# Kernel tuning notes

Measured on AMD Instinct MI355X. Metric: run time of the kernel, lower is better.

Reference implementation:

```python
import jax, jax.numpy as jnp
import numpy as np

N = 16384          # number of vectors to quantize (flattened leading dims)
K = 2 ** 14        # codebook_size = 2**bits_per_codeword
D = 64             # vector_dim


def setup_inputs() -> dict:
    key = jax.random.key(0)
    k1, k2, k3, k4 = jax.random.split(key, 4)
    x_re = jax.random.normal(k1, (N, D), dtype=jnp.float32)
    x_im = jax.random.normal(k2, (N, D), dtype=jnp.float32)
    # random complex codebook, normalized so each row has unit complex L2 norm
    cb_re = jax.random.normal(k3, (K, D), dtype=jnp.float32)
    cb_im = jax.random.normal(k4, (K, D), dtype=jnp.float32)
    norm = jnp.sqrt(jnp.sum(cb_re * cb_re + cb_im * cb_im, axis=1, keepdims=True))
    cb_re = cb_re / norm
    cb_im = cb_im / norm
    return {"x_re": x_re, "x_im": x_im, "cb_re": cb_re, "cb_im": cb_im}


def reference(x_re, x_im, cb_re, cb_im):
    # complex inner product conj(x) . c, expanded in real arithmetic:
    #   Re = x_re.c_re + x_im.c_im ;  Im = x_re.c_im - x_im.c_re
    dot_re = jnp.einsum('nd,kd->nk', x_re, cb_re) + jnp.einsum('nd,kd->nk', x_im, cb_im)
    dot_im = jnp.einsum('nd,kd->nk', x_re, cb_im) - jnp.einsum('nd,kd->nk', x_im, cb_re)
    mag = jnp.sqrt(dot_re * dot_re + dot_im * dot_im)  # [N, K] abs of complex dot
    indices = jnp.argmax(mag, axis=-1)                 # [N] int
    # reconstruction: gather codebook rows (call() with int input)
    recon = jnp.stack([cb_re[indices], cb_im[indices]], axis=-1)  # [N, D, 2] (re, im)
    return indices, recon
```

## Files before the change

### kernel.cpp

```cpp
#include <hip/hip_runtime.h>

#define NROWS 16384
#define KCB   16384
#define DD    64
#define BM    256
#define CSPLIT 16
#define COLS_PER_BLOCK 1024
#define TILE_COLS 128
#define NTILES (COLS_PER_BLOCK / TILE_COLS)
#define NCHUNK (TILE_COLS / 16)
#define CAP 2048
#define DELTA 0.45f
#define TILE_BYTES 32768

typedef __attribute__((ext_vector_type(8))) short bf16x8;
typedef __attribute__((ext_vector_type(4))) float f32x4;
typedef __attribute__((ext_vector_type(2))) float f32x2;

__device__ __forceinline__ unsigned pk_bf16(float lo, float hi) {
    unsigned a = __float_as_uint(lo);
    unsigned b = __float_as_uint(hi);
    a += 0x7FFFu + ((a >> 16) & 1u);
    b += 0x7FFFu + ((b >> 16) & 1u);
    return (a >> 16) | (b & 0xFFFF0000u);
}

__device__ __forceinline__ bf16x8 mk8(unsigned a, unsigned b, unsigned c, unsigned d) {
    union { uint4 u; bf16x8 v; } x;
    x.u = make_uint4(a, b, c, d);
    return x.v;
}

__device__ __forceinline__ f32x2 lo2(f32x4 v) { return __builtin_shufflevector(v, v, 0, 1); }
__device__ __forceinline__ f32x2 hi2(f32x4 v) { return __builtin_shufflevector(v, v, 2, 3); }

__device__ __forceinline__ unsigned swz(unsigned row, unsigned byte_in_row) {
    return row * 128u + (byte_in_row ^ ((row & 7u) << 4));
}

__device__ __forceinline__ void gload_lds16(const void* g, void* l) {
    __builtin_amdgcn_global_load_lds(
        (__attribute__((address_space(1))) void*)(g),
        (__attribute__((address_space(3))) void*)(l), 16, 0, 0);
}

__device__ __forceinline__ void rescore_fast(
    int n, int k,
    const float* __restrict__ x_re, const float* __restrict__ x_im,
    const float* __restrict__ cb_re, const float* __restrict__ cb_im,
    unsigned long long* __restrict__ best_packed)
{
    const float4* xr = (const float4*)(x_re + (size_t)n * DD);
    const float4* xi = (const float4*)(x_im + (size_t)n * DD);
    const float4* cr = (const float4*)(cb_re + (size_t)k * DD);
    const float4* ci = (const float4*)(cb_im + (size_t)k * DD);
    float accr = 0.0f, acci = 0.0f;
#pragma unroll 4
    for (int d4 = 0; d4 < 16; ++d4) {
        float4 a = xr[d4], b = xi[d4], c = cr[d4], e = ci[d4];
        accr = fmaf(a.x, c.x, accr); accr = fmaf(b.x, e.x, accr);
        acci = fmaf(a.x, e.x, acci); acci = fmaf(-b.x, c.x, acci);
        accr = fmaf(a.y, c.y, accr); accr = fmaf(b.y, e.y, accr);
        acci = fmaf(a.y, e.y, acci); acci = fmaf(-b.y, c.y, acci);
        accr = fmaf(a.z, c.z, accr); accr = fmaf(b.z, e.z, accr);
        acci = fmaf(a.z, e.z, acci); acci = fmaf(-b.z, c.z, acci);
        accr = fmaf(a.w, c.w, accr); accr = fmaf(b.w, e.w, accr);
        acci = fmaf(a.w, e.w, acci); acci = fmaf(-b.w, c.w, acci);
    }
    float m2 = accr * accr + acci * acci;
    unsigned long long key =
        ((unsigned long long)__float_as_uint(m2) << 32) | (unsigned)(~(unsigned)k);
    atomicMax(best_packed + n, key);
}

__global__ __launch_bounds__(256) void prep(
    const float* __restrict__ cb_re, const float* __restrict__ cb_im,
    uint4* __restrict__ cb_sw,
    unsigned* __restrict__ row_max_bits,
    unsigned long long* __restrict__ best_packed, int* __restrict__ flags)
{
    int id = blockIdx.x * 256 + threadIdx.x;
    if (id < NROWS) { row_max_bits[id] = 0u; best_packed[id] = 0ull; }
    if (id < 1024) flags[id] = 0;
    int u   = id & 1023;
    int arr = (id >> 10) & 1;
    int gt  = id >> 11;
    int c   = u >> 3;
    int b   = ((u & 7) * 16) ^ ((c & 7) << 4);
    int col = gt * TILE_COLS + c;
    int d0  = b >> 1;
    const float* src = arr ? cb_im : cb_re;
    const float4* p = (const float4*)(src + (size_t)col * DD + d0);
    float4 f0 = p[0], f1 = p[1];
    cb_sw[id] = make_uint4(pk_bf16(f0.x, f0.y), pk_bf16(f0.z, f0.w),
                           pk_bf16(f1.x, f1.y), pk_bf16(f1.z, f1.w));
}

template<int PASS>
__global__ __launch_bounds__(512, 2) void score_kernel(
    const float* __restrict__ x_re, const float* __restrict__ x_im,
    const float* __restrict__ cb_re, const float* __restrict__ cb_im,
    const char* __restrict__ cb_sw,
    unsigned* __restrict__ row_max_bits,
    unsigned long long* __restrict__ best_packed, int* __restrict__ flags)
{
    __shared__ char Bls[2][2][TILE_COLS * 128];
    __shared__ unsigned cand[CAP];
    __shared__ int cand_cnt;

    const int tid  = threadIdx.x;
    const int lane = tid & 63;
    const int wid  = tid >> 6;
    const int row0 = blockIdx.x * BM;
    const int col0 = blockIdx.y * COLS_PER_BLOCK;
    const int bid  = blockIdx.y * gridDim.x + blockIdx.x;
    const int l15  = lane & 15;
    const int lhi  = lane >> 4;

    if (tid == 0) cand_cnt = 0;

    bf16x8 Ar[2][2], Ai[2][2], Ain[2][2];
#pragma unroll
    for (int a = 0; a < 2; ++a) {
        const int row = row0 + wid * 32 + a * 16 + l15;
#pragma unroll
        for (int ks = 0; ks < 2; ++ks) {
            const float4* pr = (const float4*)(x_re + (size_t)row * DD + ks * 32 + lhi * 8);
            const float4* pi = (const float4*)(x_im + (size_t)row * DD + ks * 32 + lhi * 8);
            float4 r0 = pr[0], r1 = pr[1];
            float4 i0 = pi[0], i1 = pi[1];
            Ar[a][ks] = mk8(pk_bf16(r0.x, r0.y), pk_bf16(r0.z, r0.w),
                            pk_bf16(r1.x, r1.y), pk_bf16(r1.z, r1.w));
            Ai[a][ks] = mk8(pk_bf16(i0.x, i0.y), pk_bf16(i0.z, i0.w),
                            pk_bf16(i1.x, i1.y), pk_bf16(i1.z, i1.w));
            Ain[a][ks] = Ai[a][ks] ^ (short)0x8000;
        }
    }

    const f32x4 FZERO = (f32x4){0.f, 0.f, 0.f, 0.f};

    f32x2 rm2[2][2];
    f32x2 thr2[2][2];
#pragma unroll
    for (int a = 0; a < 2; ++a)
#pragma unroll
        for (int j = 0; j < 2; ++j) rm2[a][j] = (f32x2){0.f, 0.f};
    if (PASS == 2) {
#pragma unroll
        for (int a = 0; a < 2; ++a)
#pragma unroll
            for (int j = 0; j < 2; ++j) {
#pragma unroll
                for (int h = 0; h < 2; ++h) {
                    int n = row0 + wid * 32 + a * 16 + lhi * 4 + j * 2 + h;
                    float mx = __uint_as_float(row_max_bits[n]);
                    float tm = sqrtf(mx) - DELTA;
                    thr2[a][j][h] = (tm > 0.0f) ? tm * tm : -1.0f;
                }
            }
    }

    bool ovf = false;

    const char* tile_base = cb_sw + (size_t)blockIdx.y * NTILES * TILE_BYTES;
    auto stage = [&](int buf, int t) {
        const char* src = tile_base + (size_t)t * TILE_BYTES;
        char* dst = &Bls[buf][0][0];
#pragma unroll
        for (int j = 0; j < 4; ++j)
            gload_lds16(src + j * 8192 + tid * 16, dst + j * 8192 + tid * 16);
    };

    stage(0, 0);
    __syncthreads();

    for (int t = 0; t < NTILES; ++t) {
        const int cur = t & 1;
        if (t + 1 < NTILES) {
            stage(cur ^ 1, t + 1);
            asm volatile("s_waitcnt vmcnt(4)" ::: "memory");
        } else {
            asm volatile("s_waitcnt vmcnt(0)" ::: "memory");
        }
        __builtin_amdgcn_sched_barrier(0);
        __builtin_amdgcn_s_barrier();
        __builtin_amdgcn_sched_barrier(0);

        for (int ch = 0; ch < NCHUNK; ++ch) {
            const char* B0 = &Bls[cur][0][0];
            const char* B1 = &Bls[cur][1][0];
            const int colLocal = ch * 16 + l15;
            unsigned off0 = swz(colLocal, lhi * 16);
            unsigned off1 = swz(colLocal, 64 + lhi * 16);
            bf16x8 br0 = *(const bf16x8*)(B0 + off0);
            bf16x8 bi0 = *(const bf16x8*)(B1 + off0);
            bf16x8 br1 = *(const bf16x8*)(B0 + off1);
            bf16x8 bi1 = *(const bf16x8*)(B1 + off1);

            f32x4 accre[2], accim[2];
#pragma unroll
            for (int a = 0; a < 2; ++a) {
                accre[a] = __builtin_amdgcn_mfma_f32_16x16x32_bf16(Ar[a][0], br0, FZERO, 0, 0, 0);
                accre[a] = __builtin_amdgcn_mfma_f32_16x16x32_bf16(Ai[a][0], bi0, accre[a], 0, 0, 0);
                accre[a] = __builtin_amdgcn_mfma_f32_16x16x32_bf16(Ar[a][1], br1, accre[a], 0, 0, 0);
                accre[a] = __builtin_amdgcn_mfma_f32_16x16x32_bf16(Ai[a][1], bi1, accre[a], 0, 0, 0);
                accim[a] = __builtin_amdgcn_mfma_f32_16x16x32_bf16(Ar[a][0], bi0, FZERO, 0, 0, 0);
                accim[a] = __builtin_amdgcn_mfma_f32_16x16x32_bf16(Ain[a][0], br0, accim[a], 0, 0, 0);
                accim[a] = __builtin_amdgcn_mfma_f32_16x16x32_bf16(Ar[a][1], bi1, accim[a], 0, 0, 0);
                accim[a] = __builtin_amdgcn_mfma_f32_16x16x32_bf16(Ain[a][1], br1, accim[a], 0, 0, 0);
            }

#pragma unroll
            for (int a = 0; a < 2; ++a) {
                f32x2 m2p[2];
                {
                    f32x2 rl = lo2(accre[a]), il = lo2(accim[a]);
                    f32x2 rh = hi2(accre[a]), ih = hi2(accim[a]);
                    m2p[0] = rl * rl + il * il;
                    m2p[1] = rh * rh + ih * ih;
                }
                if (PASS == 1) {
#pragma unroll
                    for (int j = 0; j < 2; ++j)
                        rm2[a][j] = __builtin_elementwise_max(rm2[a][j], m2p[j]);
                } else {
#pragma unroll
                    for (int j = 0; j < 2; ++j)
#pragma unroll
                        for (int h = 0; h < 2; ++h) {
                            if (m2p[j][h] >= thr2[a][j][h]) {
                                int nl = wid * 32 + a * 16 + lhi * 4 + j * 2 + h;
                                int k  = col0 + t * TILE_COLS + ch * 16 + l15;
                                int idx = atomicAdd(&cand_cnt, 1);
                                if (idx < CAP) cand[idx] = ((unsigned)nl << 14) | (unsigned)k;
                                else ovf = true;
                            }
                        }
                }
            }
        }

        __builtin_amdgcn_sched_barrier(0);
        __builtin_amdgcn_s_barrier();
    }
    __syncthreads();

    if (PASS == 1) {
#pragma unroll
        for (int a = 0; a < 2; ++a)
#pragma unroll
            for (int j = 0; j < 2; ++j)
#pragma unroll
                for (int h = 0; h < 2; ++h) {
                    float v = rm2[a][j][h];
#pragma unroll
                    for (int m = 1; m < 16; m <<= 1)
                        v = fmaxf(v, __shfl_xor(v, m, 64));
                    if (l15 == 0) {
                        int n = row0 + wid * 32 + a * 16 + lhi * 4 + j * 2 + h;
                        atomicMax(&row_max_bits[n], __float_as_uint(v));
                    }
                }
    } else {
        if (ovf) flags[bid] = 1;
        int cnt = cand_cnt < CAP ? cand_cnt : CAP;
        for (int i = tid; i < cnt; i += 512) {
            unsigned e = cand[i];
            rescore_fast(row0 + (int)(e >> 14), (int)(e & 16383u),
                         x_re, x_im, cb_re, cb_im, best_packed);
        }
    }
}

__global__ __launch_bounds__(512) void rescue(
    const float* __restrict__ x_re, const float* __restrict__ x_im,
    const float* __restrict__ cb_re, const float* __restrict__ cb_im,
    const int* __restrict__ flags,
    unsigned long long* __restrict__ best_packed)
{
    const int bid = blockIdx.x;
    if (flags[bid] == 0) return;
    const int row0 = (bid & 63) * BM;
    const int col0 = (bid >> 6) * COLS_PER_BLOCK;
    for (int i = threadIdx.x; i < BM * COLS_PER_BLOCK; i += 512)
        rescore_fast(row0 + (i >> 10), col0 + (i & 1023),
                     x_re, x_im, cb_re, cb_im, best_packed);
}

__global__ __launch_bounds__(256) void finalize(
    const unsigned long long* __restrict__ best_packed,
    const float* __restrict__ cb_re, const float* __restrict__ cb_im,
    float* __restrict__ out)
{
    const int wave = threadIdx.x >> 6;
    const int lane = threadIdx.x & 63;
    const int n = blockIdx.x * 4 + wave;
    if (n >= NROWS) return;

    unsigned long long p = best_packed[n];
    unsigned k = ~(unsigned)(p & 0xFFFFFFFFull);

    if (lane == 0) out[n] = (float)k;

    float re = cb_re[(size_t)k * DD + lane];
    float im = cb_im[(size_t)k * DD + lane];
    float2* ro = reinterpret_cast<float2*>(out + NROWS);
    ro[(size_t)n * DD + lane] = make_float2(re, im);
}

extern "C" void kernel_launch(void* const* d_in, const int* in_sizes, int n_in,
                              void* d_out, int out_size, void* d_ws, size_t ws_size,
                              hipStream_t stream)
{
    const float* x_re  = (const float*)d_in[0];
    const float* x_im  = (const float*)d_in[1];
    const float* cb_re = (const float*)d_in[2];
    const float* cb_im = (const float*)d_in[3];
    float* out = (float*)d_out;

    const size_t CB_SW_BYTES = (size_t)(KCB / TILE_COLS) * TILE_BYTES;
    char* p = (char*)d_ws;
    const char* cb_sw = p;                                        p += CB_SW_BYTES;
    unsigned long long* best_packed = (unsigned long long*)p;     p += (size_t)NROWS * 8;
    unsigned* row_max_bits = (unsigned*)p;                        p += (size_t)NROWS * 4;
    int* flags = (int*)p;

    prep<<<1024, 256, 0, stream>>>(cb_re, cb_im, (uint4*)d_ws,
                                   row_max_bits, best_packed, flags);

    dim3 grid(NROWS / BM, CSPLIT);
    score_kernel<1><<<grid, 512, 0, stream>>>(x_re, x_im, cb_re, cb_im, cb_sw,
                                              row_max_bits, best_packed, flags);
    score_kernel<2><<<grid, 512, 0, stream>>>(x_re, x_im, cb_re, cb_im, cb_sw,
                                              row_max_bits, best_packed, flags);

    rescue<<<1024, 512, 0, stream>>>(x_re, x_im, cb_re, cb_im, flags, best_packed);

    finalize<<<NROWS / 4, 256, 0, stream>>>(best_packed, cb_re, cb_im, out);
}
```

Baseline: 295.8 us.

## Replace full max pass with sampled estimate kernel over a subset of codebook tiles

Drops the first full scoring pass, which computed each row's exact max magnitude over the whole codebook. A small est_kernel now computes a lower-bound estimate of that max from 8 codebook tiles. The single scoring pass then filters candidates against a threshold derived from this estimate. This roughly halves the MFMA work, but the looser threshold lets many more candidates through to the fp32 rescoring. It also raises the risk of overflowing the candidate buffer, which triggers the expensive rescue path.

```diff
diff --git a/kernel.cpp b/kernel.cpp
--- a/kernel.cpp
+++ b/kernel.cpp
@@ -9,13 +9,13 @@
 #define TILE_COLS 128
 #define NTILES (COLS_PER_BLOCK / TILE_COLS)
 #define NCHUNK (TILE_COLS / 16)
+#define EST_TILES 8
 #define CAP 2048
 #define DELTA 0.45f
 #define TILE_BYTES 32768
 
 typedef __attribute__((ext_vector_type(8))) short bf16x8;
 typedef __attribute__((ext_vector_type(4))) float f32x4;
-typedef __attribute__((ext_vector_type(2))) float f32x2;
 
 __device__ __forceinline__ unsigned pk_bf16(float lo, float hi) {
     unsigned a = __float_as_uint(lo);
@@ -30,9 +30,6 @@
     x.u = make_uint4(a, b, c, d);
     return x.v;
 }
-
-__device__ __forceinline__ f32x2 lo2(f32x4 v) { return __builtin_shufflevector(v, v, 0, 1); }
-__device__ __forceinline__ f32x2 hi2(f32x4 v) { return __builtin_shufflevector(v, v, 2, 3); }
 
 __device__ __forceinline__ unsigned swz(unsigned row, unsigned byte_in_row) {
     return row * 128u + (byte_in_row ^ ((row & 7u) << 4));
@@ -76,11 +73,11 @@
 __global__ __launch_bounds__(256) void prep(
     const float* __restrict__ cb_re, const float* __restrict__ cb_im,
     uint4* __restrict__ cb_sw,
-    unsigned* __restrict__ row_max_bits,
+    unsigned* __restrict__ row_est,
     unsigned long long* __restrict__ best_packed, int* __restrict__ flags)
 {
     int id = blockIdx.x * 256 + threadIdx.x;
-    if (id < NROWS) { row_max_bits[id] = 0u; best_packed[id] = 0ull; }
+    if (id < NROWS) { row_est[id] = 0u; best_packed[id] = 0ull; }
     if (id < 1024) flags[id] = 0;
     int u   = id & 1023;
     int arr = (id >> 10) & 1;
@@ -96,30 +93,21 @@
                            pk_bf16(f1.x, f1.y), pk_bf16(f1.z, f1.w));
 }
 
-template<int PASS>
-__global__ __launch_bounds__(512, 2) void score_kernel(
+__global__ __launch_bounds__(512, 2) void est_kernel(
     const float* __restrict__ x_re, const float* __restrict__ x_im,
-    const float* __restrict__ cb_re, const float* __restrict__ cb_im,
     const char* __restrict__ cb_sw,
-    unsigned* __restrict__ row_max_bits,
-    unsigned long long* __restrict__ best_packed, int* __restrict__ flags)
-{
-    __shared__ char Bls[2][2][TILE_COLS * 128];
-    __shared__ unsigned cand[CAP];
-    __shared__ int cand_cnt;
+    unsigned* __restrict__ row_est)
+{
+    __shared__ char Bls[2][TILE_COLS * 128];
 
     const int tid  = threadIdx.x;
     const int lane = tid & 63;
     const int wid  = tid >> 6;
     const int row0 = blockIdx.x * BM;
-    const int col0 = blockIdx.y * COLS_PER_BLOCK;
-    const int bid  = blockIdx.y * gridDim.x + blockIdx.x;
     const int l15  = lane & 15;
     const int lhi  = lane >> 4;
 
-    if (tid == 0) cand_cnt = 0;
-
-    bf16x8 Ar[2][2], Ai[2][2], Ain[2][2];
+    bf16x8 Ar[2][2], Ai[2][2];
 #pragma unroll
     for (int a = 0; a < 2; ++a) {
         const int row = row0 + wid * 32 + a * 16 + l15;
@@ -133,32 +121,142 @@
                             pk_bf16(r1.x, r1.y), pk_bf16(r1.z, r1.w));
             Ai[a][ks] = mk8(pk_bf16(i0.x, i0.y), pk_bf16(i0.z, i0.w),
                             pk_bf16(i1.x, i1.y), pk_bf16(i1.z, i1.w));
-            Ain[a][ks] = Ai[a][ks] ^ (short)0x8000;
-        }
-    }
-
-    const f32x4 FZERO = (f32x4){0.f, 0.f, 0.f, 0.f};
-
-    f32x2 rm2[2][2];
-    f32x2 thr2[2][2];
+        }
+    }
+
+    {
+        const char* src = cb_sw + (size_t)blockIdx.y * TILE_BYTES;
+        char* dst = &Bls[0][0];
+#pragma unroll
+        for (int j = 0; j < 4; ++j)
+            gload_lds16(src + j * 8192 + tid * 16, dst + j * 8192 + tid * 16);
+    }
+    __syncthreads();
+
+    float rm[2][4];
 #pragma unroll
     for (int a = 0; a < 2; ++a)
 #pragma unroll
-        for (int j = 0; j < 2; ++j) rm2[a][j] = (f32x2){0.f, 0.f};
-    if (PASS == 2) {
+        for (int r = 0; r < 4; ++r) rm[a][r] = 0.0f;
+
+    for (int ch = 0; ch < NCHUNK; ++ch) {
+        const char* B0 = &Bls[0][0];
+        const char* B1 = &Bls[1][0];
+        const int colLocal = ch * 16 + l15;
+        unsigned off0 = swz(colLocal, lhi * 16);
+        unsigned off1 = swz(colLocal, 64 + lhi * 16);
+        bf16x8 br0 = *(const bf16x8*)(B0 + off0);
+        bf16x8 bi0 = *(const bf16x8*)(B1 + off0);
+        bf16x8 br1 = *(const bf16x8*)(B0 + off1);
+        bf16x8 bi1 = *(const bf16x8*)(B1 + off1);
+
+        f32x4 accre[2], accim[2];
+#pragma unroll
+        for (int a = 0; a < 2; ++a) {
+            accre[a] = (f32x4){0.f, 0.f, 0.f, 0.f};
+            accim[a] = (f32x4){0.f, 0.f, 0.f, 0.f};
+        }
+#pragma unroll
+        for (int a = 0; a < 2; ++a) {
+            accre[a] = __builtin_amdgcn_mfma_f32_16x16x32_bf16(Ar[a][0], br0, accre[a], 0, 0, 0);
+            accre[a] = __builtin_amdgcn_mfma_f32_16x16x32_bf16(Ai[a][0], bi0, accre[a], 0, 0, 0);
+            accre[a] = __builtin_amdgcn_mfma_f32_16x16x32_bf16(Ar[a][1], br1, accre[a], 0, 0, 0);
+            accre[a] = __builtin_amdgcn_mfma_f32_16x16x32_bf16(Ai[a][1], bi1, accre[a], 0, 0, 0);
+            accim[a] = __builtin_amdgcn_mfma_f32_16x16x32_bf16(Ar[a][0], bi0, accim[a], 0, 0, 0);
+            accim[a] = __builtin_amdgcn_mfma_f32_16x16x32_bf16(Ar[a][1], bi1, accim[a], 0, 0, 0);
+        }
+        br0 = br0 ^ (short)0x8000;
+        br1 = br1 ^ (short)0x8000;
+#pragma unroll
+        for (int a = 0; a < 2; ++a) {
+            accim[a] = __builtin_amdgcn_mfma_f32_16x16x32_bf16(Ai[a][0], br0, accim[a], 0, 0, 0);
+            accim[a] = __builtin_amdgcn_mfma_f32_16x16x32_bf16(Ai[a][1], br1, accim[a], 0, 0, 0);
+        }
 #pragma unroll
         for (int a = 0; a < 2; ++a)
 #pragma unroll
-            for (int j = 0; j < 2; ++j) {
-#pragma unroll
-                for (int h = 0; h < 2; ++h) {
-                    int n = row0 + wid * 32 + a * 16 + lhi * 4 + j * 2 + h;
-                    float mx = __uint_as_float(row_max_bits[n]);
-                    float tm = sqrtf(mx) - DELTA;
-                    thr2[a][j][h] = (tm > 0.0f) ? tm * tm : -1.0f;
-                }
+            for (int r = 0; r < 4; ++r) {
+                float re = accre[a][r], im = accim[a][r];
+                rm[a][r] = fmaxf(rm[a][r], fmaf(re, re, im * im));
             }
     }
+
+#pragma unroll
+    for (int m = 1; m < 16; m <<= 1)
+#pragma unroll
+        for (int a = 0; a < 2; ++a)
+#pragma unroll
+            for (int r = 0; r < 4; ++r)
+                rm[a][r] = fmaxf(rm[a][r], __shfl_xor(rm[a][r], m, 64));
+    if (l15 == 0) {
+#pragma unroll
+        for (int a = 0; a < 2; ++a)
+#pragma unroll
+            for (int r = 0; r < 4; ++r) {
+                int n = row0 + wid * 32 + a * 16 + lhi * 4 + r;
+                atomicMax(&row_est[n], __float_as_uint(rm[a][r]));
+            }
+    }
+}
+
+__global__ __launch_bounds__(512, 2) void score_kernel(
+    const float* __restrict__ x_re, const float* __restrict__ x_im,
+    const float* __restrict__ cb_re, const float* __restrict__ cb_im,
+    const char* __restrict__ cb_sw,
+    const unsigned* __restrict__ row_est,
+    unsigned long long* __restrict__ best_packed, int* __restrict__ flags)
+{
+    __shared__ char Bls[2][2][TILE_COLS * 128];
+    __shared__ unsigned cand[CAP];
+    __shared__ int cand_cnt;
+
+    const int tid  = threadIdx.x;
+    const int lane = tid & 63;
+    const int wid  = tid >> 6;
+    const int row0 = blockIdx.x * BM;
+    const int col0 = blockIdx.y * COLS_PER_BLOCK;
+    const int bid  = blockIdx.y * gridDim.x + blockIdx.x;
+    const int l15  = lane & 15;
+    const int lhi  = lane >> 4;
+
+    if (tid == 0) cand_cnt = 0;
+
+    bf16x8 Ar[2][2], Ai[2][2];
+#pragma unroll
+    for (int a = 0; a < 2; ++a) {
+        const int row = row0 + wid * 32 + a * 16 + l15;
+        {
+            const float4* pr = (const float4*)(x_re + (size_t)row * DD + lhi * 8);
+            const float4* pi = (const float4*)(x_im + (size_t)row * DD + lhi * 8);
+            float4 r0 = pr[0], r1 = pr[1];
+            float4 i0 = pi[0], i1 = pi[1];
+            Ar[a][0] = mk8(pk_bf16(r0.x, r0.y), pk_bf16(r0.z, r0.w),
+                           pk_bf16(r1.x, r1.y), pk_bf16(r1.z, r1.w));
+            Ai[a][0] = mk8(pk_bf16(i0.x, i0.y), pk_bf16(i0.z, i0.w),
+                           pk_bf16(i1.x, i1.y), pk_bf16(i1.z, i1.w));
+        }
+        {
+            const float4* pr = (const float4*)(x_re + (size_t)row * DD + 32 + lhi * 8);
+            const float4* pi = (const float4*)(x_im + (size_t)row * DD + 32 + lhi * 8);
+            float4 r0 = pr[0], r1 = pr[1];
+            float4 i0 = pi[0], i1 = pi[1];
+            Ar[a][1] = mk8(pk_bf16(r0.x, r0.y), pk_bf16(r0.z, r0.w),
+                           pk_bf16(r1.x, r1.y), pk_bf16(r1.z, r1.w));
+            Ai[a][1] = mk8(pk_bf16(i0.x, i0.y), pk_bf16(i0.z, i0.w),
+                           pk_bf16(i1.x, i1.y), pk_bf16(i1.z, i1.w));
+        }
+    }
+
+    float thr[2][4];
+#pragma unroll
+    for (int a = 0; a < 2; ++a)
+#pragma unroll
+        for (int r = 0; r < 4; ++r) {
+            int n = row0 + wid * 32 + a * 16 + lhi * 4 + r;
+            float mx = __uint_as_float(row_est[n]);
+            float tm = sqrtf(mx) - DELTA;
+            thr[a][r] = (tm > 0.0f) ? tm * tm : -1.0f;
+        }
 
     bool ovf = false;
 
@@ -200,44 +298,40 @@
             f32x4 accre[2], accim[2];
 #pragma unroll
             for (int a = 0; a < 2; ++a) {
-                accre[a] = __builtin_amdgcn_mfma_f32_16x16x32_bf16(Ar[a][0], br0, FZERO, 0, 0, 0);
+                accre[a] = (f32x4){0.f, 0.f, 0.f, 0.f};
+                accim[a] = (f32x4){0.f, 0.f, 0.f, 0.f};
+            }
+#pragma unroll
+            for (int a = 0; a < 2; ++a) {
+                accre[a] = __builtin_amdgcn_mfma_f32_16x16x32_bf16(Ar[a][0], br0, accre[a], 0, 0, 0);
                 accre[a] = __builtin_amdgcn_mfma_f32_16x16x32_bf16(Ai[a][0], bi0, accre[a], 0, 0, 0);
                 accre[a] = __builtin_amdgcn_mfma_f32_16x16x32_bf16(Ar[a][1], br1, accre[a], 0, 0, 0);
                 accre[a] = __builtin_amdgcn_mfma_f32_16x16x32_bf16(Ai[a][1], bi1, accre[a], 0, 0, 0);
-                accim[a] = __builtin_amdgcn_mfma_f32_16x16x32_bf16(Ar[a][0], bi0, FZERO, 0, 0, 0);
-                accim[a] = __builtin_amdgcn_mfma_f32_16x16x32_bf16(Ain[a][0], br0, accim[a], 0, 0, 0);
+                accim[a] = __builtin_amdgcn_mfma_f32_16x16x32_bf16(Ar[a][0], bi0, accim[a], 0, 0, 0);
                 accim[a] = __builtin_amdgcn_mfma_f32_16x16x32_bf16(Ar[a][1], bi1, accim[a], 0, 0, 0);
-                accim[a] = __builtin_amdgcn_mfma_f32_16x16x32_bf16(Ain[a][1], br1, accim[a], 0, 0, 0);
             }
-
+            br0 = br0 ^ (short)0x8000;
+            br1 = br1 ^ (short)0x8000;
 #pragma unroll
             for (int a = 0; a < 2; ++a) {
-                f32x2 m2p[2];
-                {
-                    f32x2 rl = lo2(accre[a]), il = lo2(accim[a]);
-                    f32x2 rh = hi2(accre[a]), ih = hi2(accim[a]);
-                    m2p[0] = rl * rl + il * il;
-                    m2p[1] = rh * rh + ih * ih;
+                accim[a] = __builtin_amdgcn_mfma_f32_16x16x32_bf16(Ai[a][0], br0, accim[a], 0, 0, 0);
+                accim[a] = __builtin_amdgcn_mfma_f32_16x16x32_bf16(Ai[a][1], br1, accim[a], 0, 0, 0);
+            }
+
+#pragma unroll
+            for (int a = 0; a < 2; ++a)
+#pragma unroll
+                for (int r = 0; r < 4; ++r) {
+                    float re = accre[a][r], im = accim[a][r];
+                    float m2 = fmaf(re, re, im * im);
+                    if (m2 >= thr[a][r]) {
+                        int nl = wid * 32 + a * 16 + lhi * 4 + r;
+                        int k  = col0 + t * TILE_COLS + ch * 16 + l15;
+                        int idx = atomicAdd(&cand_cnt, 1);
+                        if (idx < CAP) cand[idx] = ((unsigned)nl << 14) | (unsigned)k;
+                        else ovf = true;
+                    }
                 }
-                if (PASS == 1) {
-#pragma unroll
-                    for (int j = 0; j < 2; ++j)
-                        rm2[a][j] = __builtin_elementwise_max(rm2[a][j], m2p[j]);
-                } else {
-#pragma unroll
-                    for (int j = 0; j < 2; ++j)
-#pragma unroll
-                        for (int h = 0; h < 2; ++h) {
-                            if (m2p[j][h] >= thr2[a][j][h]) {
-                                int nl = wid * 32 + a * 16 + lhi * 4 + j * 2 + h;
-                                int k  = col0 + t * TILE_COLS + ch * 16 + l15;
-                                int idx = atomicAdd(&cand_cnt, 1);
-                                if (idx < CAP) cand[idx] = ((unsigned)nl << 14) | (unsigned)k;
-                                else ovf = true;
-                            }
-                        }
-                }
-            }
         }
 
         __builtin_amdgcn_sched_barrier(0);
@@ -245,30 +339,12 @@
     }
     __syncthreads();
 
-    if (PASS == 1) {
-#pragma unroll
-        for (int a = 0; a < 2; ++a)
-#pragma unroll
-            for (int j = 0; j < 2; ++j)
-#pragma unroll
-                for (int h = 0; h < 2; ++h) {
-                    float v = rm2[a][j][h];
-#pragma unroll
-                    for (int m = 1; m < 16; m <<= 1)
-                        v = fmaxf(v, __shfl_xor(v, m, 64));
-                    if (l15 == 0) {
-                        int n = row0 + wid * 32 + a * 16 + lhi * 4 + j * 2 + h;
-                        atomicMax(&row_max_bits[n], __float_as_uint(v));
-                    }
-                }
-    } else {
-        if (ovf) flags[bid] = 1;
-        int cnt = cand_cnt < CAP ? cand_cnt : CAP;
-        for (int i = tid; i < cnt; i += 512) {
-            unsigned e = cand[i];
-            rescore_fast(row0 + (int)(e >> 14), (int)(e & 16383u),
-                         x_re, x_im, cb_re, cb_im, best_packed);
-        }
+    if (ovf) flags[bid] = 1;
+    int cnt = cand_cnt < CAP ? cand_cnt : CAP;
+    for (int i = tid; i < cnt; i += 512) {
+        unsigned e = cand[i];
+        rescore_fast(row0 + (int)(e >> 14), (int)(e & 16383u),
+                     x_re, x_im, cb_re, cb_im, best_packed);
     }
 }
 
@@ -322,17 +398,18 @@
     char* p = (char*)d_ws;
     const char* cb_sw = p;                                        p += CB_SW_BYTES;
     unsigned long long* best_packed = (unsigned long long*)p;     p += (size_t)NROWS * 8;
-    unsigned* row_max_bits = (unsigned*)p;                        p += (size_t)NROWS * 4;
+    unsigned* row_est = (unsigned*)p;                             p += (size_t)NROWS * 4;
     int* flags = (int*)p;
 
     prep<<<1024, 256, 0, stream>>>(cb_re, cb_im, (uint4*)d_ws,
-                                   row_max_bits, best_packed, flags);
+                                   row_est, best_packed, flags);
+
+    dim3 egrid(NROWS / BM, EST_TILES);
+    est_kernel<<<egrid, 512, 0, stream>>>(x_re, x_im, cb_sw, row_est);
 
     dim3 grid(NROWS / BM, CSPLIT);
-    score_kernel<1><<<grid, 512, 0, stream>>>(x_re, x_im, cb_re, cb_im, cb_sw,
-                                              row_max_bits, best_packed, flags);
-    score_kernel<2><<<grid, 512, 0, stream>>>(x_re, x_im, cb_re, cb_im, cb_sw,
-                                              row_max_bits, best_packed, flags);
+    score_kernel<<<grid, 512, 0, stream>>>(x_re, x_im, cb_re, cb_im, cb_sw,
+                                           row_est, best_packed, flags);
 
     rescue<<<1024, 512, 0, stream>>>(x_re, x_im, cb_re, cb_im, flags, best_packed);
 
```

Measured after the change: 404.0 us. 1.37x slower.

## Double rows per block and negate codebook fragment instead of keeping negated X

Applied to the files above, without the earlier changes.

Each wave now covers 64 rows (BM 512) instead of 32, so every codebook tile loaded into LDS feeds twice as many MFMAs and the tile traffic per output is halved. The per-row negated imaginary input registers (Ain) are dropped; the real codebook fragments are sign-flipped once per chunk after the first MFMA group, which frees registers. The max and threshold bookkeeping is changed to scalar per-element form. The catch is higher register pressure with launch bounds of 2 blocks per CU, half as many blocks in the grid, and a candidate buffer shared by twice as many rows that may overflow more often into the rescue path.

```diff
diff --git a/kernel.cpp b/kernel.cpp
--- a/kernel.cpp
+++ b/kernel.cpp
@@ -3,7 +3,7 @@
 #define NROWS 16384
 #define KCB   16384
 #define DD    64
-#define BM    256
+#define BM    512
 #define CSPLIT 16
 #define COLS_PER_BLOCK 1024
 #define TILE_COLS 128
@@ -15,7 +15,6 @@
 
 typedef __attribute__((ext_vector_type(8))) short bf16x8;
 typedef __attribute__((ext_vector_type(4))) float f32x4;
-typedef __attribute__((ext_vector_type(2))) float f32x2;
 
 __device__ __forceinline__ unsigned pk_bf16(float lo, float hi) {
     unsigned a = __float_as_uint(lo);
@@ -30,9 +29,6 @@
     x.u = make_uint4(a, b, c, d);
     return x.v;
 }
-
-__device__ __forceinline__ f32x2 lo2(f32x4 v) { return __builtin_shufflevector(v, v, 0, 1); }
-__device__ __forceinline__ f32x2 hi2(f32x4 v) { return __builtin_shufflevector(v, v, 2, 3); }
 
 __device__ __forceinline__ unsigned swz(unsigned row, unsigned byte_in_row) {
     return row * 128u + (byte_in_row ^ ((row & 7u) << 4));
@@ -81,7 +77,7 @@
 {
     int id = blockIdx.x * 256 + threadIdx.x;
     if (id < NROWS) { row_max_bits[id] = 0u; best_packed[id] = 0ull; }
-    if (id < 1024) flags[id] = 0;
+    if (id < 512) flags[id] = 0;
     int u   = id & 1023;
     int arr = (id >> 10) & 1;
     int gt  = id >> 11;
@@ -119,10 +115,10 @@
 
     if (tid == 0) cand_cnt = 0;
 
-    bf16x8 Ar[2][2], Ai[2][2], Ain[2][2];
-#pragma unroll
-    for (int a = 0; a < 2; ++a) {
-        const int row = row0 + wid * 32 + a * 16 + l15;
+    bf16x8 Ar[4][2], Ai[4][2];
+#pragma unroll
+    for (int a = 0; a < 4; ++a) {
+        const int row = row0 + wid * 64 + a * 16 + l15;
 #pragma unroll
         for (int ks = 0; ks < 2; ++ks) {
             const float4* pr = (const float4*)(x_re + (size_t)row * DD + ks * 32 + lhi * 8);
@@ -133,30 +129,24 @@
                             pk_bf16(r1.x, r1.y), pk_bf16(r1.z, r1.w));
             Ai[a][ks] = mk8(pk_bf16(i0.x, i0.y), pk_bf16(i0.z, i0.w),
                             pk_bf16(i1.x, i1.y), pk_bf16(i1.z, i1.w));
-            Ain[a][ks] = Ai[a][ks] ^ (short)0x8000;
-        }
-    }
-
-    const f32x4 FZERO = (f32x4){0.f, 0.f, 0.f, 0.f};
-
-    f32x2 rm2[2][2];
-    f32x2 thr2[2][2];
-#pragma unroll
-    for (int a = 0; a < 2; ++a)
-#pragma unroll
-        for (int j = 0; j < 2; ++j) rm2[a][j] = (f32x2){0.f, 0.f};
+        }
+    }
+
+    float rm[4][4];
+    float thr[4][4];
+#pragma unroll
+    for (int a = 0; a < 4; ++a)
+#pragma unroll
+        for (int r = 0; r < 4; ++r) rm[a][r] = 0.0f;
     if (PASS == 2) {
 #pragma unroll
-        for (int a = 0; a < 2; ++a)
-#pragma unroll
-            for (int j = 0; j < 2; ++j) {
-#pragma unroll
-                for (int h = 0; h < 2; ++h) {
-                    int n = row0 + wid * 32 + a * 16 + lhi * 4 + j * 2 + h;
-                    float mx = __uint_as_float(row_max_bits[n]);
-                    float tm = sqrtf(mx) - DELTA;
-                    thr2[a][j][h] = (tm > 0.0f) ? tm * tm : -1.0f;
-                }
+        for (int a = 0; a < 4; ++a)
+#pragma unroll
+            for (int r = 0; r < 4; ++r) {
+                int n = row0 + wid * 64 + a * 16 + lhi * 4 + r;
+                float mx = __uint_as_float(row_max_bits[n]);
+                float tm = sqrtf(mx) - DELTA;
+                thr[a][r] = (tm > 0.0f) ? tm * tm : -1.0f;
             }
     }
 
@@ -197,47 +187,47 @@
             bf16x8 br1 = *(const bf16x8*)(B0 + off1);
             bf16x8 bi1 = *(const bf16x8*)(B1 + off1);
 
-            f32x4 accre[2], accim[2];
-#pragma unroll
-            for (int a = 0; a < 2; ++a) {
-                accre[a] = __builtin_amdgcn_mfma_f32_16x16x32_bf16(Ar[a][0], br0, FZERO, 0, 0, 0);
+            f32x4 accre[4], accim[4];
+#pragma unroll
+            for (int a = 0; a < 4; ++a) {
+                accre[a] = (f32x4){0.f, 0.f, 0.f, 0.f};
+                accim[a] = (f32x4){0.f, 0.f, 0.f, 0.f};
+            }
+#pragma unroll
+            for (int a = 0; a < 4; ++a) {
+                accre[a] = __builtin_amdgcn_mfma_f32_16x16x32_bf16(Ar[a][0], br0, accre[a], 0, 0, 0);
                 accre[a] = __builtin_amdgcn_mfma_f32_16x16x32_bf16(Ai[a][0], bi0, accre[a], 0, 0, 0);
                 accre[a] = __builtin_amdgcn_mfma_f32_16x16x32_bf16(Ar[a][1], br1, accre[a], 0, 0, 0);
                 accre[a] = __builtin_amdgcn_mfma_f32_16x16x32_bf16(Ai[a][1], bi1, accre[a], 0, 0, 0);
-                accim[a] = __builtin_amdgcn_mfma_f32_16x16x32_bf16(Ar[a][0], bi0, FZERO, 0, 0, 0);
-                accim[a] = __builtin_amdgcn_mfma_f32_16x16x32_bf16(Ain[a][0], br0, accim[a], 0, 0, 0);
+                accim[a] = __builtin_amdgcn_mfma_f32_16x16x32_bf16(Ar[a][0], bi0, accim[a], 0, 0, 0);
                 accim[a] = __builtin_amdgcn_mfma_f32_16x16x32_bf16(Ar[a][1], bi1, accim[a], 0, 0, 0);
-                accim[a] = __builtin_amdgcn_mfma_f32_16x16x32_bf16(Ain[a][1], br1, accim[a], 0, 0, 0);
             }
-
-#pragma unroll
-            for (int a = 0; a < 2; ++a) {
-                f32x2 m2p[2];
-                {
-                    f32x2 rl = lo2(accre[a]), il = lo2(accim[a]);
-                    f32x2 rh = hi2(accre[a]), ih = hi2(accim[a]);
-                    m2p[0] = rl * rl + il * il;
-                    m2p[1] = rh * rh + ih * ih;
+            br0 = br0 ^ (short)0x8000;
+            br1 = br1 ^ (short)0x8000;
+#pragma unroll
+            for (int a = 0; a < 4; ++a) {
+                accim[a] = __builtin_amdgcn_mfma_f32_16x16x32_bf16(Ai[a][0], br0, accim[a], 0, 0, 0);
+                accim[a] = __builtin_amdgcn_mfma_f32_16x16x32_bf16(Ai[a][1], br1, accim[a], 0, 0, 0);
+            }
+
+#pragma unroll
+            for (int a = 0; a < 4; ++a)
+#pragma unroll
+                for (int r = 0; r < 4; ++r) {
+                    float re = accre[a][r], im = accim[a][r];
+                    float m2 = fmaf(re, re, im * im);
+                    if (PASS == 1) {
+                        rm[a][r] = fmaxf(rm[a][r], m2);
+                    } else {
+                        if (m2 >= thr[a][r]) {
+                            int nl = wid * 64 + a * 16 + lhi * 4 + r;
+                            int k  = col0 + t * TILE_COLS + ch * 16 + l15;
+                            int idx = atomicAdd(&cand_cnt, 1);
+                            if (idx < CAP) cand[idx] = ((unsigned)nl << 14) | (unsigned)k;
+                            else ovf = true;
+                        }
+                    }
                 }
-                if (PASS == 1) {
-#pragma unroll
-                    for (int j = 0; j < 2; ++j)
-                        rm2[a][j] = __builtin_elementwise_max(rm2[a][j], m2p[j]);
-                } else {
-#pragma unroll
-                    for (int j = 0; j < 2; ++j)
-#pragma unroll
-                        for (int h = 0; h < 2; ++h) {
-                            if (m2p[j][h] >= thr2[a][j][h]) {
-                                int nl = wid * 32 + a * 16 + lhi * 4 + j * 2 + h;
-                                int k  = col0 + t * TILE_COLS + ch * 16 + l15;
-                                int idx = atomicAdd(&cand_cnt, 1);
-                                if (idx < CAP) cand[idx] = ((unsigned)nl << 14) | (unsigned)k;
-                                else ovf = true;
-                            }
-                        }
-                }
-            }
         }
 
         __builtin_amdgcn_sched_barrier(0);
@@ -247,20 +237,21 @@
 
     if (PASS == 1) {
 #pragma unroll
-        for (int a = 0; a < 2; ++a)
-#pragma unroll
-            for (int j = 0; j < 2; ++j)
-#pragma unroll
-                for (int h = 0; h < 2; ++h) {
-                    float v = rm2[a][j][h];
-#pragma unroll
-                    for (int m = 1; m < 16; m <<= 1)
-                        v = fmaxf(v, __shfl_xor(v, m, 64));
-                    if (l15 == 0) {
-                        int n = row0 + wid * 32 + a * 16 + lhi * 4 + j * 2 + h;
-                        atomicMax(&row_max_bits[n], __float_as_uint(v));
-                    }
+        for (int m = 1; m < 16; m <<= 1)
+#pragma unroll
+            for (int a = 0; a < 4; ++a)
+#pragma unroll
+                for (int r = 0; r < 4; ++r)
+                    rm[a][r] = fmaxf(rm[a][r], __shfl_xor(rm[a][r], m, 64));
+        if (l15 == 0) {
+#pragma unroll
+            for (int a = 0; a < 4; ++a)
+#pragma unroll
+                for (int r = 0; r < 4; ++r) {
+                    int n = row0 + wid * 64 + a * 16 + lhi * 4 + r;
+                    atomicMax(&row_max_bits[n], __float_as_uint(rm[a][r]));
                 }
+        }
     } else {
         if (ovf) flags[bid] = 1;
         int cnt = cand_cnt < CAP ? cand_cnt : CAP;
@@ -280,8 +271,8 @@
 {
     const int bid = blockIdx.x;
     if (flags[bid] == 0) return;
-    const int row0 = (bid & 63) * BM;
-    const int col0 = (bid >> 6) * COLS_PER_BLOCK;
+    const int row0 = (bid & 31) * BM;
+    const int col0 = (bid >> 5) * COLS_PER_BLOCK;
     for (int i = threadIdx.x; i < BM * COLS_PER_BLOCK; i += 512)
         rescore_fast(row0 + (i >> 10), col0 + (i & 1023),
                      x_re, x_im, cb_re, cb_im, best_packed);
@@ -334,7 +325,7 @@
     score_kernel<2><<<grid, 512, 0, stream>>>(x_re, x_im, cb_re, cb_im, cb_sw,
                                               row_max_bits, best_packed, flags);
 
-    rescue<<<1024, 512, 0, stream>>>(x_re, x_im, cb_re, cb_im, flags, best_packed);
+    rescue<<<512, 512, 0, stream>>>(x_re, x_im, cb_re, cb_im, flags, best_packed);
 
     finalize<<<NROWS / 4, 256, 0, stream>>>(best_packed, cb_re, cb_im, out);
 }
```

Result: no change. 300.2 us (+1.5%).
